# Performance work log

Measured on AMD Instinct MI355X. Metric: run time of the kernel, lower is better.

The kernel has to match this reference:

```python
import jax, jax.numpy as jnp
import numpy as np

B, N, D = 8, 2048, 512


def setup_inputs() -> dict:
    key = jax.random.key(0)
    ks = jax.random.split(key, 5)
    bound = 1.0 / np.sqrt(D)
    return {
        "query": jax.random.normal(ks[0], (B, N, D), dtype=jnp.float32),
        "context": jax.random.normal(ks[1], (B, N, D), dtype=jnp.float32),
        "Wq": jax.random.uniform(ks[2], (D, D), minval=-bound, maxval=bound, dtype=jnp.float32),
        "bq": jnp.zeros((D,), dtype=jnp.float32),
        "Wv": jax.random.uniform(ks[3], (D, D), minval=-bound, maxval=bound, dtype=jnp.float32),
        "bv": jnp.zeros((D,), dtype=jnp.float32),
        "Wo": jax.random.uniform(ks[4], (D, D), minval=-bound, maxval=bound, dtype=jnp.float32),
        "bo": jnp.zeros((D,), dtype=jnp.float32),
    }


def reference(query, context, Wq, bq, Wv, bv, Wo, bo):
    d = query.shape[-1]
    scale = 1.0 / jnp.sqrt(jnp.asarray(d, dtype=query.dtype))
    # Linear projections (eqx.nn.Linear: y = W @ x + b -> x @ W.T + b)
    q = jnp.einsum("bnd,ed->bne", query, Wq) + bq      # (B, N, D)
    v = jnp.einsum("bnd,ed->bne", context, Wv) + bv    # (B, N, D)
    # NOTE: original module computes scores against RAW context (key layer unused)
    scores = jnp.einsum("bqd,bkd->bqk", q, context) * scale  # (B, N, N)
    attn = jax.nn.softmax(scores, axis=-1)
    h = jnp.einsum("bqk,bkd->bqd", attn, v)            # (B, N, D)
    return jnp.einsum("bnd,ed->bne", h, Wo) + bo
```

## Files before the change

### kernel.cpp

```cpp
#include <hip/hip_runtime.h>
#include <math.h>

#define NB  8
#define SEQ 2048
#define DIM 512

typedef short v8s __attribute__((ext_vector_type(8)));
typedef float v4f __attribute__((ext_vector_type(4)));

__device__ __forceinline__ unsigned short f2bf(float f) {
    unsigned int u = __float_as_uint(f);
    u += 0x7fffu + ((u >> 16) & 1u);
    return (unsigned short)(u >> 16);
}
__device__ __forceinline__ float bf2f(unsigned short h) {
    return __uint_as_float((unsigned int)h << 16);
}
__device__ __forceinline__ void async16(const unsigned short* g, unsigned short* l) {
    __builtin_amdgcn_global_load_lds(
        (const __attribute__((address_space(1))) unsigned int*)g,
        (__attribute__((address_space(3))) unsigned int*)l, 16, 0, 0);
}

__global__ __launch_bounds__(256)
void conv_bf16(const float* __restrict__ x, unsigned short* __restrict__ y)
{
    int i = blockIdx.x * 256 + threadIdx.x;
    float4 v = ((const float4*)x)[i];
    ushort4 o; o.x = f2bf(v.x); o.y = f2bf(v.y); o.z = f2bf(v.z); o.w = f2bf(v.w);
    ((ushort4*)y)[i] = o;
}

template<int MODE>
__global__ __launch_bounds__(256, 2)
void proj_sgl(const unsigned short* __restrict__ Xbf, const float* __restrict__ W,
              const float* __restrict__ bias, unsigned short* __restrict__ Y)
{
    __shared__ __align__(16) unsigned short As[128 * 64];
    __shared__ __align__(16) unsigned short Bs[128 * 64];

    const int t = threadIdx.x, wave = t >> 6, lane = t & 63;
    const int l15 = lane & 15, quad = lane >> 4;
    const int m0 = blockIdx.x * 128, e0 = blockIdx.y * 128;

    v4f hacc[2][8];
#pragma unroll
    for (int mt = 0; mt < 2; mt++)
#pragma unroll
        for (int nt = 0; nt < 8; nt++) hacc[mt][nt] = (v4f){0.f, 0.f, 0.f, 0.f};

    const int lr8 = lane >> 3, lc8 = lane & 7;

#define STAGE_A(bk)                                                            \
    _Pragma("unroll") for (int i = 0; i < 4; i++) {                            \
        int row = wave * 32 + i * 8 + lr8;                                     \
        int lc = lc8 ^ (row & 7);                                              \
        async16(Xbf + (size_t)(m0 + row) * DIM + (bk) * 64 + lc * 8,           \
                &As[(wave * 32 + i * 8) * 64]);                                \
    }
#define STAGE_B(bk)                                                            \
    _Pragma("unroll") for (int j = 0; j < 8; j++) {                            \
        int u = t * 8 + j;                                                     \
        int row = u >> 4, c4 = u & 15;                                         \
        float4 wv = *(const float4*)(W + (size_t)(e0 + row) * DIM + (bk) * 64 + c4 * 4); \
        ushort4 o = make_ushort4(f2bf(wv.x), f2bf(wv.y), f2bf(wv.z), f2bf(wv.w)); \
        int sc = (c4 >> 1) ^ (row & 7);                                        \
        *(ushort4*)&Bs[row * 64 + sc * 8 + (c4 & 1) * 4] = o;                  \
    }

    STAGE_A(0) STAGE_B(0)
    for (int bk = 0; bk < 8; bk++) {
        __syncthreads();
#pragma unroll
        for (int kc = 0; kc < 2; kc++) {
            v8s a[2];
#pragma unroll
            for (int mt = 0; mt < 2; mt++) {
                int row = wave * 32 + mt * 16 + l15;
                a[mt] = *(const v8s*)&As[row * 64 + (((kc * 4 + quad) ^ (row & 7)) * 8)];
            }
#pragma unroll
            for (int nt = 0; nt < 8; nt++) {
                int er = nt * 16 + l15;
                v8s bfr = *(const v8s*)&Bs[er * 64 + (((kc * 4 + quad) ^ (er & 7)) * 8)];
#pragma unroll
                for (int mt = 0; mt < 2; mt++)
                    hacc[mt][nt] = __builtin_amdgcn_mfma_f32_16x16x32_bf16(a[mt], bfr, hacc[mt][nt], 0, 0, 0);
            }
        }
        __syncthreads();
        if (bk + 1 < 8) { STAGE_A(bk + 1) STAGE_B(bk + 1) }
    }
#undef STAGE_A
#undef STAGE_B

#pragma unroll
    for (int mt = 0; mt < 2; mt++)
#pragma unroll
        for (int nt = 0; nt < 8; nt++) {
            int col = e0 + nt * 16 + l15;
            float bb = bias[col];
            if (MODE == 0) {
#pragma unroll
                for (int r = 0; r < 4; r++) {
                    int row = m0 + wave * 32 + mt * 16 + quad * 4 + r;
                    Y[(size_t)row * DIM + col] = f2bf(hacc[mt][nt][r] + bb);
                }
            } else {
                int rowb = m0 + wave * 32 + mt * 16 + quad * 4;
                int bidx = rowb >> 11, n = rowb & 2047;
                ushort4 o = make_ushort4(f2bf(hacc[mt][nt][0] + bb), f2bf(hacc[mt][nt][1] + bb),
                                         f2bf(hacc[mt][nt][2] + bb), f2bf(hacc[mt][nt][3] + bb));
                *(ushort4*)&Y[(size_t)bidx * DIM * SEQ + (size_t)col * SEQ + n] = o;
            }
        }
}

__global__ __launch_bounds__(256, 2)
void proj_split(const unsigned short* __restrict__ Ahi, const unsigned short* __restrict__ Alo,
                const float* __restrict__ W, const float* __restrict__ bias,
                float* __restrict__ Y)
{
    __shared__ __align__(16) unsigned short Ah[128 * 64];
    __shared__ __align__(16) unsigned short Al[128 * 64];
    __shared__ __align__(16) unsigned short Bh[128 * 64];
    __shared__ __align__(16) unsigned short Bl[128 * 64];

    const int t = threadIdx.x, wave = t >> 6, lane = t & 63;
    const int l15 = lane & 15, quad = lane >> 4;
    const int m0 = blockIdx.x * 128, e0 = blockIdx.y * 128;

    v4f hacc[2][8];
#pragma unroll
    for (int mt = 0; mt < 2; mt++)
#pragma unroll
        for (int nt = 0; nt < 8; nt++) hacc[mt][nt] = (v4f){0.f, 0.f, 0.f, 0.f};

    const int lr8 = lane >> 3, lc8 = lane & 7;

#define STAGE_A2(bk)                                                           \
    _Pragma("unroll") for (int i = 0; i < 4; i++) {                            \
        int row = wave * 32 + i * 8 + lr8;                                     \
        int lc = lc8 ^ (row & 7);                                              \
        size_t ga = (size_t)(m0 + row) * DIM + (bk) * 64 + lc * 8;             \
        async16(Ahi + ga, &Ah[(wave * 32 + i * 8) * 64]);                      \
        async16(Alo + ga, &Al[(wave * 32 + i * 8) * 64]);                      \
    }
#define STAGE_B2(bk)                                                           \
    _Pragma("unroll") for (int j = 0; j < 8; j++) {                            \
        int u = t * 8 + j;                                                     \
        int row = u >> 4, c4 = u & 15;                                         \
        float4 wv = *(const float4*)(W + (size_t)(e0 + row) * DIM + (bk) * 64 + c4 * 4); \
        ushort4 oh = make_ushort4(f2bf(wv.x), f2bf(wv.y), f2bf(wv.z), f2bf(wv.w)); \
        ushort4 ol = make_ushort4(f2bf(wv.x - bf2f(oh.x)), f2bf(wv.y - bf2f(oh.y)), \
                                  f2bf(wv.z - bf2f(oh.z)), f2bf(wv.w - bf2f(oh.w))); \
        int sc = (c4 >> 1) ^ (row & 7);                                        \
        int sa = row * 64 + sc * 8 + (c4 & 1) * 4;                             \
        *(ushort4*)&Bh[sa] = oh;                                               \
        *(ushort4*)&Bl[sa] = ol;                                               \
    }

    STAGE_A2(0) STAGE_B2(0)
    for (int bk = 0; bk < 8; bk++) {
        __syncthreads();
#pragma unroll
        for (int kc = 0; kc < 2; kc++) {
            v8s ah[2], al[2];
#pragma unroll
            for (int mt = 0; mt < 2; mt++) {
                int row = wave * 32 + mt * 16 + l15;
                int sa = row * 64 + (((kc * 4 + quad) ^ (row & 7)) * 8);
                ah[mt] = *(const v8s*)&Ah[sa];
                al[mt] = *(const v8s*)&Al[sa];
            }
#pragma unroll
            for (int nt = 0; nt < 8; nt++) {
                int er = nt * 16 + l15;
                int sb = er * 64 + (((kc * 4 + quad) ^ (er & 7)) * 8);
                v8s bh = *(const v8s*)&Bh[sb];
                v8s bl = *(const v8s*)&Bl[sb];
#pragma unroll
                for (int mt = 0; mt < 2; mt++) {
                    hacc[mt][nt] = __builtin_amdgcn_mfma_f32_16x16x32_bf16(ah[mt], bh, hacc[mt][nt], 0, 0, 0);
                    hacc[mt][nt] = __builtin_amdgcn_mfma_f32_16x16x32_bf16(al[mt], bh, hacc[mt][nt], 0, 0, 0);
                    hacc[mt][nt] = __builtin_amdgcn_mfma_f32_16x16x32_bf16(ah[mt], bl, hacc[mt][nt], 0, 0, 0);
                }
            }
        }
        __syncthreads();
        if (bk + 1 < 8) { STAGE_A2(bk + 1) STAGE_B2(bk + 1) }
    }
#undef STAGE_A2
#undef STAGE_B2

#pragma unroll
    for (int mt = 0; mt < 2; mt++)
#pragma unroll
        for (int nt = 0; nt < 8; nt++) {
            int col = e0 + nt * 16 + l15;
            float bb = bias[col];
#pragma unroll
            for (int r = 0; r < 4; r++) {
                int row = m0 + wave * 32 + mt * 16 + quad * 4 + r;
                Y[(size_t)row * DIM + col] = hacc[mt][nt][r] + bb;
            }
        }
}

__global__ __launch_bounds__(512, 2)
void flash_mfma4(const unsigned short* __restrict__ qbf,
                 const unsigned short* __restrict__ ctxbf,
                 const unsigned short* __restrict__ vT,
                 unsigned short* __restrict__ hhi,
                 unsigned short* __restrict__ hlo)
{
    __shared__ __align__(16) unsigned short Ks[64 * 512];
    __shared__ __align__(16) unsigned short Ps[64 * 64];
    __shared__ float Mp[2][64];
    __shared__ float Sp[2][64];
    __shared__ float alphaS[64];

    const int t = threadIdx.x;
    const int wave = t >> 6, lane = t & 63;
    const int l15 = lane & 15, quad = lane >> 4;
    const int strip = wave & 3, half = wave >> 2;
    const int qrow0 = strip * 16 + quad * 4;
    const int b = blockIdx.x, m0 = blockIdx.y * 64;

    const unsigned short* ctxb = ctxbf + (size_t)b * SEQ * DIM;
    const unsigned short* vTb  = vT    + (size_t)b * DIM * SEQ;
    const float scale = 0.044194173824159216f;

    v8s qf[16];
    {
        const unsigned short* qrow = qbf + ((size_t)b * SEQ + m0 + strip * 16 + l15) * DIM;
#pragma unroll
        for (int kc = 0; kc < 16; kc++)
            qf[kc] = *(const v8s*)(qrow + kc * 32 + quad * 8);
    }
    v4f hacc[4][4];
#pragma unroll
    for (int m = 0; m < 4; m++)
#pragma unroll
        for (int dt = 0; dt < 4; dt++) hacc[m][dt] = (v4f){0.f, 0.f, 0.f, 0.f};

    float M[4], L[4];
#pragma unroll
    for (int r = 0; r < 4; r++) { M[r] = -INFINITY; L[r] = 0.f; }

#pragma unroll
    for (int i = 0; i < 8; i++) {
        int row = wave * 8 + i;
        async16(ctxb + (size_t)row * DIM + (size_t)(lane ^ (row & 7)) * 8, &Ks[row * 512]);
    }

    for (int kt = 0; kt < SEQ / 64; kt++) {
        __syncthreads();
        v4f sacc[2];
        sacc[0] = (v4f){0.f, 0.f, 0.f, 0.f};
        sacc[1] = (v4f){0.f, 0.f, 0.f, 0.f};
        __builtin_amdgcn_s_setprio(1);
#pragma unroll
        for (int kc = 0; kc < 16; kc++) {
#pragma unroll
            for (int ct = 0; ct < 2; ct++) {
                int key = half * 32 + ct * 16 + l15;
                v8s kf = *(const v8s*)&Ks[key * 512 + (((kc * 4 + quad) ^ (key & 7)) * 8)];
                sacc[ct] = __builtin_amdgcn_mfma_f32_16x16x32_bf16(qf[kc], kf, sacc[ct], 0, 0, 0);
            }
        }
        __builtin_amdgcn_s_setprio(0);
        float s0[4], s1[4], mx[4];
#pragma unroll
        for (int r = 0; r < 4; r++) {
            s0[r] = sacc[0][r] * scale;
            s1[r] = sacc[1][r] * scale;
            mx[r] = fmaxf(s0[r], s1[r]);
        }
#pragma unroll
        for (int off = 1; off < 16; off <<= 1)
#pragma unroll
            for (int r = 0; r < 4; r++)
                mx[r] = fmaxf(mx[r], __shfl_xor(mx[r], off, 64));
        if (l15 == 0) {
#pragma unroll
            for (int r = 0; r < 4; r++) Mp[half][qrow0 + r] = mx[r];
        }
        __syncthreads();
        float Mn[4], al[4], sm[4];
#pragma unroll
        for (int r = 0; r < 4; r++) {
            float mo = fmaxf(Mp[0][qrow0 + r], Mp[1][qrow0 + r]);
            Mn[r] = fmaxf(M[r], mo);
            al[r] = __expf(M[r] - Mn[r]);
            float p0 = __expf(s0[r] - Mn[r]);
            float p1 = __expf(s1[r] - Mn[r]);
            sm[r] = p0 + p1;
            int row = qrow0 + r;
            int k0 = half * 32 + l15;
            int k1 = k0 + 16;
            Ps[row * 64 + (((k0 >> 3) ^ (row & 7)) << 3) + (k0 & 7)] = f2bf(p0);
            Ps[row * 64 + (((k1 >> 3) ^ (row & 7)) << 3) + (k1 & 7)] = f2bf(p1);
        }
#pragma unroll
        for (int off = 1; off < 16; off <<= 1)
#pragma unroll
            for (int r = 0; r < 4; r++)
                sm[r] += __shfl_xor(sm[r], off, 64);
        if (l15 == 0) {
#pragma unroll
            for (int r = 0; r < 4; r++) Sp[half][qrow0 + r] = sm[r];
            if (half == 0) {
#pragma unroll
                for (int r = 0; r < 4; r++) alphaS[qrow0 + r] = al[r];
            }
        }
        __syncthreads();
#pragma unroll
        for (int r = 0; r < 4; r++) {
            L[r] = L[r] * al[r] + Sp[0][qrow0 + r] + Sp[1][qrow0 + r];
            M[r] = Mn[r];
        }
        if (kt + 1 < SEQ / 64) {
#pragma unroll
            for (int i = 0; i < 8; i++) {
                int row = wave * 8 + i;
                async16(ctxb + (size_t)((kt + 1) * 64 + row) * DIM + (size_t)(lane ^ (row & 7)) * 8,
                        &Ks[row * 512]);
            }
        }
        v8s vf[4][2];
#pragma unroll
        for (int dt = 0; dt < 4; dt++)
#pragma unroll
            for (int kc2 = 0; kc2 < 2; kc2++)
                vf[dt][kc2] = *(const v8s*)(vTb + (size_t)(wave * 64 + dt * 16 + l15) * SEQ
                                            + kt * 64 + kc2 * 32 + quad * 8);
#pragma unroll
        for (int m = 0; m < 4; m++) {
            v4f a4;
#pragma unroll
            for (int r = 0; r < 4; r++) a4[r] = alphaS[m * 16 + quad * 4 + r];
#pragma unroll
            for (int dt = 0; dt < 4; dt++) hacc[m][dt] *= a4;
        }
        __builtin_amdgcn_s_setprio(1);
#pragma unroll
        for (int kc2 = 0; kc2 < 2; kc2++)
#pragma unroll
            for (int m = 0; m < 4; m++) {
                int row = m * 16 + l15;
                v8s pa = *(const v8s*)&Ps[row * 64 + (((kc2 * 4 + quad) ^ (row & 7)) << 3)];
#pragma unroll
                for (int dt = 0; dt < 4; dt++)
                    hacc[m][dt] = __builtin_amdgcn_mfma_f32_16x16x32_bf16(pa, vf[dt][kc2], hacc[m][dt], 0, 0, 0);
            }
        __builtin_amdgcn_s_setprio(0);
    }

    __syncthreads();
    if (half == 0 && l15 == 0) {
#pragma unroll
        for (int r = 0; r < 4; r++) alphaS[qrow0 + r] = 1.0f / L[r];
    }
    __syncthreads();
#pragma unroll
    for (int m = 0; m < 4; m++) {
#pragma unroll
        for (int r = 0; r < 4; r++) {
            float invL = alphaS[m * 16 + quad * 4 + r];
            int grow = m0 + m * 16 + quad * 4 + r;
#pragma unroll
            for (int dt = 0; dt < 4; dt++) {
                float o = hacc[m][dt][r] * invL;
                unsigned short hi = f2bf(o);
                float lof = o - bf2f(hi);
                size_t idx = ((size_t)b * SEQ + grow) * DIM + wave * 64 + dt * 16 + l15;
                hhi[idx] = hi;
                hlo[idx] = f2bf(lof);
            }
        }
    }
}

extern "C" void kernel_launch(void* const* d_in, const int* in_sizes, int n_in,
                              void* d_out, int out_size, void* d_ws, size_t ws_size,
                              hipStream_t stream)
{
    const float* query   = (const float*)d_in[0];
    const float* context = (const float*)d_in[1];
    const float* Wq      = (const float*)d_in[2];
    const float* bq      = (const float*)d_in[3];
    const float* Wv      = (const float*)d_in[4];
    const float* bv      = (const float*)d_in[5];
    const float* Wo      = (const float*)d_in[6];
    const float* bo      = (const float*)d_in[7];

    const size_t NE = (size_t)NB * SEQ * DIM;
    unsigned short* qbf = (unsigned short*)d_ws;
    unsigned short* cbf = qbf + NE;
    unsigned short* hhi = cbf + NE;
    unsigned short* hlo = hhi + NE;
    unsigned short* vTb = (unsigned short*)d_out;
    unsigned short* qx  = ((unsigned short*)d_out) + NE;

    dim3 gridP(128, 4);

    conv_bf16   <<<NE / 1024, 256, 0, stream>>>(query, qx);
    conv_bf16   <<<NE / 1024, 256, 0, stream>>>(context, cbf);
    proj_sgl<0> <<<gridP, 256, 0, stream>>>(qx,  Wq, bq, qbf);
    proj_sgl<1> <<<gridP, 256, 0, stream>>>(cbf, Wv, bv, vTb);
    flash_mfma4 <<<dim3(NB, SEQ / 64), 512, 0, stream>>>(qbf, cbf, vTb, hhi, hlo);
    proj_split  <<<gridP, 256, 0, stream>>>(hhi, hlo, Wo, bo, (float*)d_out);
}
```

Baseline: 389.2 us.

## Halve flash attention query tile to 32 rows, split keys across four waves

The flash kernel now handles 32 query rows per block instead of 64. The 8 waves are split as 2 query strips by 4 key quarters of the 64-key tile, with max and sum reductions across four partial buffers. This doubles the grid to 512 blocks, which improves CU occupancy and load balance. The cost is that each context K tile and the V data are reloaded twice as often overall, so arithmetic intensity per byte loaded drops.

```diff
diff --git a/kernel.cpp b/kernel.cpp
--- a/kernel.cpp
+++ b/kernel.cpp
@@ -208,24 +208,24 @@
 }
 
 __global__ __launch_bounds__(512, 2)
-void flash_mfma4(const unsigned short* __restrict__ qbf,
+void flash_mfma5(const unsigned short* __restrict__ qbf,
                  const unsigned short* __restrict__ ctxbf,
                  const unsigned short* __restrict__ vT,
                  unsigned short* __restrict__ hhi,
                  unsigned short* __restrict__ hlo)
 {
     __shared__ __align__(16) unsigned short Ks[64 * 512];
-    __shared__ __align__(16) unsigned short Ps[64 * 64];
-    __shared__ float Mp[2][64];
-    __shared__ float Sp[2][64];
-    __shared__ float alphaS[64];
+    __shared__ __align__(16) unsigned short Ps[32 * 64];
+    __shared__ float Mp[4][32];
+    __shared__ float Sp[4][32];
+    __shared__ float alphaS[32];
 
     const int t = threadIdx.x;
     const int wave = t >> 6, lane = t & 63;
     const int l15 = lane & 15, quad = lane >> 4;
-    const int strip = wave & 3, half = wave >> 2;
+    const int strip = wave & 1, kq = wave >> 1;
     const int qrow0 = strip * 16 + quad * 4;
-    const int b = blockIdx.x, m0 = blockIdx.y * 64;
+    const int b = blockIdx.x, m0 = blockIdx.y * 32;
 
     const unsigned short* ctxb = ctxbf + (size_t)b * SEQ * DIM;
     const unsigned short* vTb  = vT    + (size_t)b * DIM * SEQ;
@@ -238,9 +238,9 @@
         for (int kc = 0; kc < 16; kc++)
             qf[kc] = *(const v8s*)(qrow + kc * 32 + quad * 8);
     }
-    v4f hacc[4][4];
-#pragma unroll
-    for (int m = 0; m < 4; m++)
+    v4f hacc[2][4];
+#pragma unroll
+    for (int m = 0; m < 2; m++)
 #pragma unroll
         for (int dt = 0; dt < 4; dt++) hacc[m][dt] = (v4f){0.f, 0.f, 0.f, 0.f};
 
@@ -256,26 +256,20 @@
 
     for (int kt = 0; kt < SEQ / 64; kt++) {
         __syncthreads();
-        v4f sacc[2];
-        sacc[0] = (v4f){0.f, 0.f, 0.f, 0.f};
-        sacc[1] = (v4f){0.f, 0.f, 0.f, 0.f};
+        v4f sacc = (v4f){0.f, 0.f, 0.f, 0.f};
         __builtin_amdgcn_s_setprio(1);
 #pragma unroll
         for (int kc = 0; kc < 16; kc++) {
-#pragma unroll
-            for (int ct = 0; ct < 2; ct++) {
-                int key = half * 32 + ct * 16 + l15;
-                v8s kf = *(const v8s*)&Ks[key * 512 + (((kc * 4 + quad) ^ (key & 7)) * 8)];
-                sacc[ct] = __builtin_amdgcn_mfma_f32_16x16x32_bf16(qf[kc], kf, sacc[ct], 0, 0, 0);
-            }
+            int key = kq * 16 + l15;
+            v8s kf = *(const v8s*)&Ks[key * 512 + (((kc * 4 + quad) ^ (key & 7)) * 8)];
+            sacc = __builtin_amdgcn_mfma_f32_16x16x32_bf16(qf[kc], kf, sacc, 0, 0, 0);
         }
         __builtin_amdgcn_s_setprio(0);
-        float s0[4], s1[4], mx[4];
+        float s[4], mx[4];
 #pragma unroll
         for (int r = 0; r < 4; r++) {
-            s0[r] = sacc[0][r] * scale;
-            s1[r] = sacc[1][r] * scale;
-            mx[r] = fmaxf(s0[r], s1[r]);
+            s[r] = sacc[r] * scale;
+            mx[r] = s[r];
         }
 #pragma unroll
         for (int off = 1; off < 16; off <<= 1)
@@ -284,23 +278,20 @@
                 mx[r] = fmaxf(mx[r], __shfl_xor(mx[r], off, 64));
         if (l15 == 0) {
 #pragma unroll
-            for (int r = 0; r < 4; r++) Mp[half][qrow0 + r] = mx[r];
+            for (int r = 0; r < 4; r++) Mp[kq][qrow0 + r] = mx[r];
         }
         __syncthreads();
         float Mn[4], al[4], sm[4];
 #pragma unroll
         for (int r = 0; r < 4; r++) {
-            float mo = fmaxf(Mp[0][qrow0 + r], Mp[1][qrow0 + r]);
+            int row = qrow0 + r;
+            float mo = fmaxf(fmaxf(Mp[0][row], Mp[1][row]), fmaxf(Mp[2][row], Mp[3][row]));
             Mn[r] = fmaxf(M[r], mo);
             al[r] = __expf(M[r] - Mn[r]);
-            float p0 = __expf(s0[r] - Mn[r]);
-            float p1 = __expf(s1[r] - Mn[r]);
-            sm[r] = p0 + p1;
-            int row = qrow0 + r;
-            int k0 = half * 32 + l15;
-            int k1 = k0 + 16;
-            Ps[row * 64 + (((k0 >> 3) ^ (row & 7)) << 3) + (k0 & 7)] = f2bf(p0);
-            Ps[row * 64 + (((k1 >> 3) ^ (row & 7)) << 3) + (k1 & 7)] = f2bf(p1);
+            float p = __expf(s[r] - Mn[r]);
+            sm[r] = p;
+            int k = kq * 16 + l15;
+            Ps[row * 64 + (((k >> 3) ^ (row & 7)) << 3) + (k & 7)] = f2bf(p);
         }
 #pragma unroll
         for (int off = 1; off < 16; off <<= 1)
@@ -309,8 +300,8 @@
                 sm[r] += __shfl_xor(sm[r], off, 64);
         if (l15 == 0) {
 #pragma unroll
-            for (int r = 0; r < 4; r++) Sp[half][qrow0 + r] = sm[r];
-            if (half == 0) {
+            for (int r = 0; r < 4; r++) Sp[kq][qrow0 + r] = sm[r];
+            if (kq == 0) {
 #pragma unroll
                 for (int r = 0; r < 4; r++) alphaS[qrow0 + r] = al[r];
             }
@@ -318,7 +309,8 @@
         __syncthreads();
 #pragma unroll
         for (int r = 0; r < 4; r++) {
-            L[r] = L[r] * al[r] + Sp[0][qrow0 + r] + Sp[1][qrow0 + r];
+            int row = qrow0 + r;
+            L[r] = L[r] * al[r] + (Sp[0][row] + Sp[1][row]) + (Sp[2][row] + Sp[3][row]);
             M[r] = Mn[r];
         }
         if (kt + 1 < SEQ / 64) {
@@ -337,7 +329,7 @@
                 vf[dt][kc2] = *(const v8s*)(vTb + (size_t)(wave * 64 + dt * 16 + l15) * SEQ
                                             + kt * 64 + kc2 * 32 + quad * 8);
 #pragma unroll
-        for (int m = 0; m < 4; m++) {
+        for (int m = 0; m < 2; m++) {
             v4f a4;
 #pragma unroll
             for (int r = 0; r < 4; r++) a4[r] = alphaS[m * 16 + quad * 4 + r];
@@ -348,7 +340,7 @@
 #pragma unroll
         for (int kc2 = 0; kc2 < 2; kc2++)
 #pragma unroll
-            for (int m = 0; m < 4; m++) {
+            for (int m = 0; m < 2; m++) {
                 int row = m * 16 + l15;
                 v8s pa = *(const v8s*)&Ps[row * 64 + (((kc2 * 4 + quad) ^ (row & 7)) << 3)];
 #pragma unroll
@@ -359,13 +351,13 @@
     }
 
     __syncthreads();
-    if (half == 0 && l15 == 0) {
+    if (kq == 0 && l15 == 0) {
 #pragma unroll
         for (int r = 0; r < 4; r++) alphaS[qrow0 + r] = 1.0f / L[r];
     }
     __syncthreads();
 #pragma unroll
-    for (int m = 0; m < 4; m++) {
+    for (int m = 0; m < 2; m++) {
 #pragma unroll
         for (int r = 0; r < 4; r++) {
             float invL = alphaS[m * 16 + quad * 4 + r];
@@ -410,6 +402,6 @@
     conv_bf16   <<<NE / 1024, 256, 0, stream>>>(context, cbf);
     proj_sgl<0> <<<gridP, 256, 0, stream>>>(qx,  Wq, bq, qbf);
     proj_sgl<1> <<<gridP, 256, 0, stream>>>(cbf, Wv, bv, vTb);
-    flash_mfma4 <<<dim3(NB, SEQ / 64), 512, 0, stream>>>(qbf, cbf, vTb, hhi, hlo);
+    flash_mfma5 <<<dim3(NB, SEQ / 32), 512, 0, stream>>>(qbf, cbf, vTb, hhi, hlo);
     proj_split  <<<gridP, 256, 0, stream>>>(hhi, hlo, Wo, bo, (float*)d_out);
 }
```

After: 510.3 us. 1.31x slower.
